# Performance work log

Measured on AMD Instinct MI355X. Metric: run time of the kernel, lower is better.

## Reference

```python
import jax, jax.numpy as jnp
import numpy as np

HEADS = 16
D_MODEL = 1024
GROUP = 4
SEQ = 2048
HEAD_DIM = D_MODEL // HEADS          # 64
KV_HEADS = HEADS // GROUP            # 4


def rope_tables(head_dim, seq_len, base=10000.0):
    # NOTE: faithful to source: exp = -2*arange(0,d,2)/d  (steps of 2 -> base^{-4j/d})
    exp = -2.0 * jnp.arange(0, head_dim, 2, dtype=jnp.float32) / head_dim
    thetas = jnp.power(base, exp)                       # [d/2]
    m = jnp.arange(seq_len, dtype=jnp.float32)          # [S]
    freq = jnp.outer(m, thetas)                         # [S, d/2]
    return jnp.cos(freq), jnp.sin(freq)


def apply_rope(x, cos, sin):
    # x: [B,S,H,D]; complex rotation on consecutive pairs
    B, S, H, D = x.shape
    xr = x.reshape(B, S, H, D // 2, 2)
    x0, x1 = xr[..., 0], xr[..., 1]
    c = cos[None, :S, None, :]
    s = sin[None, :S, None, :]
    out = jnp.stack([x0 * c - x1 * s, x0 * s + x1 * c], axis=-1)
    return out.reshape(B, S, H, D)


def setup_inputs() -> dict:
    key = jax.random.key(0)
    ks = jax.random.split(key, 8)
    B = 1
    q = jax.random.normal(ks[0], (B, SEQ, D_MODEL), dtype=jnp.float32)
    k = jax.random.normal(ks[1], (B, SEQ, D_MODEL), dtype=jnp.float32)
    v = jax.random.normal(ks[2], (B, SEQ, D_MODEL), dtype=jnp.float32)
    mask = jnp.tril(jnp.ones((SEQ, SEQ), dtype=jnp.int32))[None]  # causal [B,S,S]
    sc = 0.02
    Wq = jax.random.normal(ks[3], (D_MODEL, D_MODEL), dtype=jnp.float32) * sc
    Wk = jax.random.normal(ks[4], (D_MODEL, D_MODEL // GROUP), dtype=jnp.float32) * sc
    Wv = jax.random.normal(ks[5], (D_MODEL, D_MODEL // GROUP), dtype=jnp.float32) * sc
    Wo = jax.random.normal(ks[6], (D_MODEL, D_MODEL), dtype=jnp.float32) * sc
    bq = jnp.zeros((D_MODEL,), jnp.float32)
    bk = jnp.zeros((D_MODEL // GROUP,), jnp.float32)
    bv = jnp.zeros((D_MODEL // GROUP,), jnp.float32)
    bo = jnp.zeros((D_MODEL,), jnp.float32)
    return {"q": q, "k": k, "v": v, "mask": mask, "Wq": Wq, "bq": bq,
            "Wk": Wk, "bk": bk, "Wv": Wv, "bv": bv, "Wo": Wo, "bo": bo}


def reference(q, k, v, mask, Wq, bq, Wk, bk, Wv, bv, Wo, bo):
    B, S, _ = q.shape
    cos, sin = rope_tables(HEAD_DIM, S)
    qh = (q @ Wq + bq).reshape(B, S, HEADS, HEAD_DIM)
    kh = (k @ Wk + bk).reshape(B, S, KV_HEADS, HEAD_DIM)
    vh = (v @ Wv + bv).reshape(B, S, KV_HEADS, HEAD_DIM)
    qh = apply_rope(qh, cos, sin)
    kh = apply_rope(kh, cos, sin)
    qh = qh.transpose(0, 2, 1, 3)                       # [B,H,S,D]
    kh = kh.transpose(0, 2, 1, 3)                       # [B,Hkv,S,D]
    vh = vh.transpose(0, 2, 1, 3)
    # torch .repeat tiles: query head j attends kv head j % KV_HEADS
    kh = jnp.tile(kh, (1, GROUP, 1, 1))                 # [B,H,S,D]
    vh = jnp.tile(vh, (1, GROUP, 1, 1))
    scores = jnp.einsum('bhqd,bhkd->bhqk', qh, kh) / jnp.sqrt(
        jnp.asarray(HEAD_DIM, dtype=qh.dtype))
    scores = jnp.where(mask[:, None, :, :] == 0, -jnp.inf, scores)
    attn = jax.nn.softmax(scores, axis=-1)
    out = jnp.einsum('bhqk,bhkd->bhqd', attn, vh)
    out = out.transpose(0, 2, 1, 3).reshape(B, S, D_MODEL)
    return out @ Wo + bo
```

## Files before the change

### kernel.cpp

```cpp
#include <hip/hip_runtime.h>
#include <hip/hip_bf16.h>
#include <math.h>


#define SEQ 2048
#define DM 1024
#define HD 64

using u16 = unsigned short;
typedef __attribute__((ext_vector_type(8))) short bf16x8;
typedef __attribute__((ext_vector_type(4))) float f32x4;

#define QSCALE 0.18033688011112042f

__device__ __forceinline__ u16 f2b(float f) {
    union { float f; unsigned int i; } v; v.f = f;
    unsigned int u = v.i;
    return (u16)((u + 0x7fffu + ((u >> 16) & 1u)) >> 16);
}
__device__ __forceinline__ u16 f2b_fast(float f) {
    union { float f; unsigned int i; } v; v.f = f;
    return (u16)((v.i + 0x8000u) >> 16);
}

__global__ __launch_bounds__(256) void prep_kernel(
    const float* __restrict__ qin, const float* __restrict__ kin, const float* __restrict__ vin,
    const float* __restrict__ Wq, const float* __restrict__ Wk,
    const float* __restrict__ Wv, const float* __restrict__ Wo,
    u16* __restrict__ Xq, u16* __restrict__ Xk, u16* __restrict__ Xv,
    u16* __restrict__ Wt, u16* __restrict__ wot, float2* __restrict__ rope)
{
    const int b = blockIdx.x;
    const int t = threadIdx.x;

    if (b < 640) {
        __shared__ short T[64][72];
        const float* W; u16* dst; int N, t0, rowoff;
        if (b < 256)      { W = Wq; dst = Wt;  N = 1024; t0 = b;       rowoff = 0; }
        else if (b < 320) { W = Wk; dst = Wt;  N = 256;  t0 = b - 256; rowoff = 1024; }
        else if (b < 384) { W = Wv; dst = Wt;  N = 256;  t0 = b - 320; rowoff = 1280; }
        else              { W = Wo; dst = wot; N = 1024; t0 = b - 384; rowoff = 0; }
        const int ntn = N >> 6;
        const int k0 = (t0 / ntn) * 64, n0 = (t0 % ntn) * 64;
        const int r = t >> 4, c4 = (t & 15) * 4;
        #pragma unroll
        for (int rr = 0; rr < 4; ++rr) {
            const int k = r + rr * 16;
            float4 w4 = *reinterpret_cast<const float4*>(W + (size_t)(k0 + k) * N + n0 + c4);
            T[c4 + 0][k] = (short)f2b(w4.x);
            T[c4 + 1][k] = (short)f2b(w4.y);
            T[c4 + 2][k] = (short)f2b(w4.z);
            T[c4 + 3][k] = (short)f2b(w4.w);
        }
        __syncthreads();
        const int n = t >> 2, ck = (t & 3) * 16;
        if (b < 384) {
            const int nt = (rowoff + n0) >> 6, kt = k0 >> 6;
            char* dp = (char*)(dst + (size_t)(nt * 16 + kt) * 4096) + n * 128;
            const int g0 = (t & 3) * 2, rx = n & 7;
            *reinterpret_cast<bf16x8*>(dp + (((g0    ) ^ rx) << 4)) =
                *reinterpret_cast<const bf16x8*>(&T[n][ck]);
            *reinterpret_cast<bf16x8*>(dp + (((g0 + 1) ^ rx) << 4)) =
                *reinterpret_cast<const bf16x8*>(&T[n][ck + 8]);
        } else {
            u16* dp = dst + (size_t)(n0 + n) * DM + k0 + ck;
            *reinterpret_cast<bf16x8*>(dp)     = *reinterpret_cast<const bf16x8*>(&T[n][ck]);
            *reinterpret_cast<bf16x8*>(dp + 8) = *reinterpret_cast<const bf16x8*>(&T[n][ck + 8]);
        }
    } else if (b < 1408) {
        const int idx = b - 640;
        const int which = idx >> 8;
        const int ib = idx & 255;
        const float* src = (which == 0) ? qin : (which == 1) ? kin : vin;
        u16* dst = (which == 0) ? Xq : (which == 1) ? Xk : Xv;
        const int m  = ib * 8 + (t >> 5);
        const int mt = m >> 6, r = m & 63, rx = r & 7;
        const int col0 = (t & 31) * 32;
        const float* sp = src + (size_t)m * 1024 + col0;
        #pragma unroll
        for (int c = 0; c < 4; ++c) {
            float4 x0 = *reinterpret_cast<const float4*>(sp + c * 8);
            float4 x1 = *reinterpret_cast<const float4*>(sp + c * 8 + 4);
            bf16x8 o;
            o[0] = (short)f2b(x0.x); o[1] = (short)f2b(x0.y);
            o[2] = (short)f2b(x0.z); o[3] = (short)f2b(x0.w);
            o[4] = (short)f2b(x1.x); o[5] = (short)f2b(x1.y);
            o[6] = (short)f2b(x1.z); o[7] = (short)f2b(x1.w);
            const int col = col0 + c * 8;
            const int kt = col >> 6, g = (col & 63) >> 3;
            char* dp = (char*)(dst + (size_t)(mt * 16 + kt) * 4096)
                     + r * 128 + ((g ^ rx) << 4);
            *reinterpret_cast<bf16x8*>(dp) = o;
        }
    } else {
        const int m = (b - 1408) * 256 + t;
        float2* rp = rope + (size_t)m * 32;
        for (int pi = 0; pi < 32; ++pi) {
            const float theta = exp2f(-0.8304820237f * (float)pi);
            float sn, cs;
            sincosf((float)m * theta, &sn, &cs);
            rp[pi] = make_float2(cs, sn);
        }
    }
}

__global__ __launch_bounds__(256) void proj_mfma(
    const u16* __restrict__ Xq, const u16* __restrict__ Xk, const u16* __restrict__ Xv,
    const u16* __restrict__ Wt,
    const float* __restrict__ bq, const float* __restrict__ bk, const float* __restrict__ bv,
    const float2* __restrict__ rope,
    u16* __restrict__ Qr, u16* __restrict__ Kr, u16* __restrict__ Vrt)
{
    const int n0 = blockIdx.x * 64, m0 = blockIdx.y * 64;
    const int zone = (n0 < 1024) ? 0 : (n0 < 1280) ? 1 : 2;
    const u16* __restrict__ Az = (zone == 0) ? Xq : (zone == 1) ? Xk : Xv;

    __shared__ __align__(16) u16 As[2][4096];
    __shared__ __align__(16) u16 Bs[2][4096];

    const int t = threadIdx.x;
    const int w = t >> 6, lane = t & 63, lm = lane & 15, quad = lane >> 4;

    f32x4 acc[4] = { {0,0,0,0}, {0,0,0,0}, {0,0,0,0}, {0,0,0,0} };

    const char* Ag = (const char*)(Az + (size_t)(m0 >> 6) * 16 * 4096);
    const char* Bg = (const char*)(Wt + (size_t)(n0 >> 6) * 16 * 4096);

    auto stage = [&](int bufi, int kti) {
        const char* gA = Ag + (size_t)kti * 8192 + w * 2048 + lane * 16;
        const char* gB = Bg + (size_t)kti * 8192 + w * 2048 + lane * 16;
        char* lA = (char*)&As[bufi][0] + w * 2048;
        char* lB = (char*)&Bs[bufi][0] + w * 2048;
        #pragma unroll
        for (int i = 0; i < 2; ++i) {
            __builtin_amdgcn_global_load_lds(
                (const __attribute__((address_space(1))) unsigned int*)(gA + i * 1024),
                (__attribute__((address_space(3))) unsigned int*)(lA + i * 1024), 16, 0, 0);
            __builtin_amdgcn_global_load_lds(
                (const __attribute__((address_space(1))) unsigned int*)(gB + i * 1024),
                (__attribute__((address_space(3))) unsigned int*)(lB + i * 1024), 16, 0, 0);
        }
    };

    stage(0, 0);
    __syncthreads();

    const int rA = 16 * w + lm;
    const int axr = rA & 7;
    for (int kt = 0; kt < 16; ++kt) {
        const int buf = kt & 1;
        if (kt < 15) stage(buf ^ 1, kt + 1);
        const char* Ab = (const char*)&As[buf][0];
        const char* Bb = (const char*)&Bs[buf][0];
        bf16x8 af0 = *reinterpret_cast<const bf16x8*>(Ab + rA * 128 + (((quad    ) ^ axr) << 4));
        bf16x8 af1 = *reinterpret_cast<const bf16x8*>(Ab + rA * 128 + (((4 | quad) ^ axr) << 4));
        #pragma unroll
        for (int nb = 0; nb < 4; ++nb) {
            const int rB = 16 * nb + lm, bxr = rB & 7;
            bf16x8 b0 = *reinterpret_cast<const bf16x8*>(Bb + rB * 128 + (((quad    ) ^ bxr) << 4));
            bf16x8 b1 = *reinterpret_cast<const bf16x8*>(Bb + rB * 128 + (((4 | quad) ^ bxr) << 4));
            acc[nb] = __builtin_amdgcn_mfma_f32_16x16x32_bf16(af0, b0, acc[nb], 0, 0, 0);
            acc[nb] = __builtin_amdgcn_mfma_f32_16x16x32_bf16(af1, b1, acc[nb], 0, 0, 0);
        }
        __syncthreads();
    }

    const float* __restrict__ bias = (zone == 0) ? bq : (zone == 1) ? bk : bv;
    const int nbase = (zone == 0) ? n0 : (zone == 1) ? (n0 - 1024) : (n0 - 1280);
    const int head = nbase >> 6;
    #pragma unroll
    for (int nb = 0; nb < 4; ++nb) {
        const int d = 16 * nb + lm;
        const float bvv = bias[nbase + d];
        float vals[4];
        #pragma unroll
        for (int r = 0; r < 4; ++r) vals[r] = acc[nb][r] + bvv;
        if (zone != 2) {
            const int pi = d >> 1;
            const bool odd = (lm & 1);
            const float sca = (zone == 0) ? QSCALE : 1.0f;
            u16* op = (zone == 0 ? Qr : Kr) + (size_t)head * SEQ * HD;
            #pragma unroll
            for (int r = 0; r < 4; ++r) {
                const int m = m0 + 16 * w + quad * 4 + r;
                const float2 cs2 = rope[(size_t)m * 32 + pi];
                float x  = vals[r];
                float xp = __shfl_xor(x, 1);
                float o  = (odd ? (xp * cs2.y + x * cs2.x)
                                : (x * cs2.x - xp * cs2.y)) * sca;
                op[(size_t)m * HD + d] = f2b(o);
            }
        } else {
            u16* vp = Vrt + ((size_t)head * HD + d) * SEQ;
            #pragma unroll
            for (int r = 0; r < 4; ++r) {
                const int m = m0 + 16 * w + quad * 4 + r;
                const int within = m & 63;
                const int pos = (m & ~63) + 4 * (within & 15) + (within >> 4);
                vp[pos] = f2b(vals[r]);
            }
        }
    }
}

__global__ __launch_bounds__(256) void attn_mfma(
    const u16* __restrict__ Qr, const u16* __restrict__ Kr, const u16* __restrict__ Vrt,
    u16* __restrict__ AO)
{
    const int bid = blockIdx.x;
    const int h  = bid & 15;
    const int qt = (bid < 256) ? (bid >> 4) : 31 - ((bid - 256) >> 4);
    const int kvh = h & 3;

    __shared__ u16 Ks[2][64][72];
    __shared__ u16 Vt[2][64][72];
    __shared__ u16 Ps[4][16][76];

    const int t = threadIdx.x;
    const int w = t >> 6, lane = t & 63, lm = lane & 15, quad = lane >> 4;

    {
        const int row = lane >> 2, c = (lane & 3) * 16;
        const u16* qp = Qr + ((size_t)h * SEQ + qt * 64 + w * 16 + row) * HD + c;
        *reinterpret_cast<bf16x8*>(&Ps[w][row][c])     = *reinterpret_cast<const bf16x8*>(qp);
        *reinterpret_cast<bf16x8*>(&Ps[w][row][c + 8]) = *reinterpret_cast<const bf16x8*>(qp + 8);
    }
    const bf16x8 aq0 = *reinterpret_cast<const bf16x8*>(&Ps[w][lm][quad * 8]);
    const bf16x8 aq1 = *reinterpret_cast<const bf16x8*>(&Ps[w][lm][32 + quad * 8]);

    f32x4 O[4] = { {0,0,0,0}, {0,0,0,0}, {0,0,0,0}, {0,0,0,0} };
    float lp[4] = { 0.f, 0.f, 0.f, 0.f };

    const int srow = t >> 2, sc2 = (t & 3) * 16;
    const u16* kb_ = Kr  + ((size_t)kvh * SEQ + srow) * HD + sc2;
    const u16* vb_ = Vrt + ((size_t)kvh * HD + srow) * SEQ + sc2;
    bf16x8 kR0 = *reinterpret_cast<const bf16x8*>(kb_);
    bf16x8 kR1 = *reinterpret_cast<const bf16x8*>(kb_ + 8);
    bf16x8 vR0 = *reinterpret_cast<const bf16x8*>(vb_);
    bf16x8 vR1 = *reinterpret_cast<const bf16x8*>(vb_ + 8);

    for (int kt = 0; kt <= qt; ++kt) {
        const int buf = kt & 1;
        *reinterpret_cast<bf16x8*>(&Ks[buf][srow][sc2])     = kR0;
        *reinterpret_cast<bf16x8*>(&Ks[buf][srow][sc2 + 8]) = kR1;
        *reinterpret_cast<bf16x8*>(&Vt[buf][srow][sc2])     = vR0;
        *reinterpret_cast<bf16x8*>(&Vt[buf][srow][sc2 + 8]) = vR1;
        if (kt < qt) {
            kR0 = *reinterpret_cast<const bf16x8*>(kb_ + (size_t)(kt + 1) * 64 * HD);
            kR1 = *reinterpret_cast<const bf16x8*>(kb_ + (size_t)(kt + 1) * 64 * HD + 8);
            vR0 = *reinterpret_cast<const bf16x8*>(vb_ + (size_t)(kt + 1) * 64);
            vR1 = *reinterpret_cast<const bf16x8*>(vb_ + (size_t)(kt + 1) * 64 + 8);
        }
        __syncthreads();

        f32x4 s[4];
        #pragma unroll
        for (int nb = 0; nb < 4; ++nb) {
            bf16x8 b0 = *reinterpret_cast<const bf16x8*>(&Ks[buf][16 * nb + lm][quad * 8]);
            bf16x8 b1 = *reinterpret_cast<const bf16x8*>(&Ks[buf][16 * nb + lm][32 + quad * 8]);
            f32x4 zz = { 0.f, 0.f, 0.f, 0.f };
            zz = __builtin_amdgcn_mfma_f32_16x16x32_bf16(aq0, b0, zz, 0, 0, 0);
            s[nb] = __builtin_amdgcn_mfma_f32_16x16x32_bf16(aq1, b1, zz, 0, 0, 0);
        }

        if (kt == qt) {
            #pragma unroll
            for (int nb = 0; nb < 4; ++nb)
                #pragma unroll
                for (int r = 0; r < 4; ++r)
                    if (16 * nb + lm > 16 * w + quad * 4 + r) s[nb][r] = -INFINITY;
        }

        #pragma unroll
        for (int r = 0; r < 4; ++r) {
            u16 pk[4];
            #pragma unroll
            for (int nb = 0; nb < 4; ++nb) {
                float e = __builtin_amdgcn_exp2f(fminf(s[nb][r], 126.f));
                lp[r] += e;
                pk[nb] = f2b_fast(e);
            }
            *reinterpret_cast<uint2*>(&Ps[w][quad * 4 + r][4 * lm]) =
                *reinterpret_cast<uint2*>(pk);
        }

        const bf16x8 ap0 = *reinterpret_cast<const bf16x8*>(&Ps[w][lm][quad * 8]);
        const bf16x8 ap1 = *reinterpret_cast<const bf16x8*>(&Ps[w][lm][32 + quad * 8]);
        #pragma unroll
        for (int db = 0; db < 4; ++db) {
            bf16x8 v0 = *reinterpret_cast<const bf16x8*>(&Vt[buf][16 * db + lm][quad * 8]);
            bf16x8 v1 = *reinterpret_cast<const bf16x8*>(&Vt[buf][16 * db + lm][32 + quad * 8]);
            O[db] = __builtin_amdgcn_mfma_f32_16x16x32_bf16(ap0, v0, O[db], 0, 0, 0);
            O[db] = __builtin_amdgcn_mfma_f32_16x16x32_bf16(ap1, v1, O[db], 0, 0, 0);
        }
    }

    #pragma unroll
    for (int r = 0; r < 4; ++r) {
        #pragma unroll
        for (int off = 1; off < 16; off <<= 1)
            lp[r] += __shfl_xor(lp[r], off);
        const float inv = 1.0f / lp[r];
        const size_t row = (size_t)(qt * 64 + 16 * w + quad * 4 + r) * DM + (size_t)h * HD;
        #pragma unroll
        for (int db = 0; db < 4; ++db)
            AO[row + 16 * db + lm] = f2b(O[db][r] * inv);
    }
}

__global__ __launch_bounds__(256) void oproj_mfma(
    const u16* __restrict__ AO, const u16* __restrict__ wot,
    const float* __restrict__ bo, float* __restrict__ out)
{
    __shared__ short As[2][64][72];
    __shared__ short Bs[2][64][72];
    const int t = threadIdx.x;
    const int w = t >> 6, lane = t & 63, lm = lane & 15, quad = lane >> 4;
    const int m0 = blockIdx.y * 64, n0 = blockIdx.x * 64;
    const int sr = t >> 2, sc = (t & 3) * 16;

    f32x4 acc[4] = { {0,0,0,0}, {0,0,0,0}, {0,0,0,0}, {0,0,0,0} };

    const u16* ap_ = AO  + (size_t)(m0 + sr) * DM + sc;
    const u16* bp_ = wot + (size_t)(n0 + sr) * DM + sc;
    bf16x8 aR0 = *reinterpret_cast<const bf16x8*>(ap_);
    bf16x8 aR1 = *reinterpret_cast<const bf16x8*>(ap_ + 8);
    bf16x8 bR0 = *reinterpret_cast<const bf16x8*>(bp_);
    bf16x8 bR1 = *reinterpret_cast<const bf16x8*>(bp_ + 8);

    for (int k0 = 0; k0 < DM; k0 += 64) {
        const int buf = (k0 >> 6) & 1;
        *reinterpret_cast<bf16x8*>(&As[buf][sr][sc])     = aR0;
        *reinterpret_cast<bf16x8*>(&As[buf][sr][sc + 8]) = aR1;
        *reinterpret_cast<bf16x8*>(&Bs[buf][sr][sc])     = bR0;
        *reinterpret_cast<bf16x8*>(&Bs[buf][sr][sc + 8]) = bR1;
        if (k0 + 64 < DM) {
            aR0 = *reinterpret_cast<const bf16x8*>(ap_ + k0 + 64);
            aR1 = *reinterpret_cast<const bf16x8*>(ap_ + k0 + 72);
            bR0 = *reinterpret_cast<const bf16x8*>(bp_ + k0 + 64);
            bR1 = *reinterpret_cast<const bf16x8*>(bp_ + k0 + 72);
        }
        __syncthreads();
        bf16x8 af0 = *reinterpret_cast<const bf16x8*>(&As[buf][16 * w + lm][quad * 8]);
        bf16x8 af1 = *reinterpret_cast<const bf16x8*>(&As[buf][16 * w + lm][32 + quad * 8]);
        #pragma unroll
        for (int nb = 0; nb < 4; ++nb) {
            bf16x8 b0 = *reinterpret_cast<const bf16x8*>(&Bs[buf][16 * nb + lm][quad * 8]);
            bf16x8 b1 = *reinterpret_cast<const bf16x8*>(&Bs[buf][16 * nb + lm][32 + quad * 8]);
            acc[nb] = __builtin_amdgcn_mfma_f32_16x16x32_bf16(af0, b0, acc[nb], 0, 0, 0);
            acc[nb] = __builtin_amdgcn_mfma_f32_16x16x32_bf16(af1, b1, acc[nb], 0, 0, 0);
        }
        __syncthreads();
    }

    #pragma unroll
    for (int nb = 0; nb < 4; ++nb) {
        const int dl = 16 * nb + lm;
        const float bv = bo[n0 + dl];
        #pragma unroll
        for (int r = 0; r < 4; ++r) {
            const int m = m0 + 16 * w + quad * 4 + r;
            out[(size_t)m * DM + n0 + dl] = acc[nb][r] + bv;
        }
    }
}

extern "C" void kernel_launch(void* const* d_in, const int* in_sizes, int n_in,
                              void* d_out, int out_size, void* d_ws, size_t ws_size,
                              hipStream_t stream)
{
    const float* q  = (const float*)d_in[0];
    const float* k  = (const float*)d_in[1];
    const float* v  = (const float*)d_in[2];
    const float* Wq = (const float*)d_in[4];
    const float* bq = (const float*)d_in[5];
    const float* Wk = (const float*)d_in[6];
    const float* bk = (const float*)d_in[7];
    const float* Wv = (const float*)d_in[8];
    const float* bv = (const float*)d_in[9];
    const float* Wo = (const float*)d_in[10];
    const float* bo = (const float*)d_in[11];
    float* out = (float*)d_out;

    u16* Xq  = (u16*)d_ws;
    u16* Xk  = Xq  + (size_t)SEQ * DM;
    u16* Xv  = Xk  + (size_t)SEQ * DM;
    u16* Wt  = Xv  + (size_t)SEQ * DM;
    u16* wot = Wt  + (size_t)1536 * 1024;
    u16* Qr  = wot + (size_t)1024 * 1024;
    u16* Kr  = Qr  + (size_t)16 * SEQ * HD;
    u16* Vrt = Kr  + (size_t)4 * SEQ * HD;
    u16* AO  = Vrt + (size_t)4 * SEQ * HD;
    float2* rope = (float2*)(AO + (size_t)SEQ * DM);

    hipLaunchKernelGGL(prep_kernel, dim3(1416), dim3(256), 0, stream,
                       q, k, v, Wq, Wk, Wv, Wo, Xq, Xk, Xv, Wt, wot, rope);
    hipLaunchKernelGGL(proj_mfma, dim3(24, 32), dim3(256), 0, stream,
                       Xq, Xk, Xv, Wt, bq, bk, bv, rope, Qr, Kr, Vrt);
    hipLaunchKernelGGL(attn_mfma, dim3(512), dim3(256), 0, stream,
                       Qr, Kr, Vrt, AO);
    hipLaunchKernelGGL(oproj_mfma, dim3(16, 32), dim3(256), 0, stream,
                       AO, wot, bo, out);
}
```

Measured before the change: 165.4 us.

## Fuse four kernels into one persistent kernel with software grid barriers

```diff
diff --git a/kernel.cpp b/kernel.cpp
--- a/kernel.cpp
+++ b/kernel.cpp
@@ -23,344 +23,362 @@
     return (u16)((v.i + 0x8000u) >> 16);
 }
 
-__global__ __launch_bounds__(256) void prep_kernel(
+__device__ __forceinline__ void gbar(unsigned int* bar, int id, int nb) {
+    __syncthreads();
+    if (threadIdx.x == 0) {
+        __threadfence();
+        unsigned int a = atomicAdd(&bar[id], 1u);
+        if (a == (unsigned int)(nb - 1)) {
+            atomicExch(&bar[id + 8], 1u);
+        } else {
+            while (atomicAdd(&bar[id + 8], 0u) == 0u)
+                __builtin_amdgcn_s_sleep(2);
+        }
+        __threadfence();
+    }
+    __syncthreads();
+}
+
+__global__ __launch_bounds__(256) void gqa_fused(
     const float* __restrict__ qin, const float* __restrict__ kin, const float* __restrict__ vin,
     const float* __restrict__ Wq, const float* __restrict__ Wk,
     const float* __restrict__ Wv, const float* __restrict__ Wo,
+    const float* __restrict__ bq, const float* __restrict__ bk,
+    const float* __restrict__ bv, const float* __restrict__ bo,
+    float* __restrict__ out,
     u16* __restrict__ Xq, u16* __restrict__ Xk, u16* __restrict__ Xv,
-    u16* __restrict__ Wt, u16* __restrict__ wot, float2* __restrict__ rope)
+    u16* __restrict__ Wt, u16* __restrict__ wot,
+    u16* __restrict__ Qr, u16* __restrict__ Kr, u16* __restrict__ Vrt,
+    u16* __restrict__ AO, float2* __restrict__ rope, unsigned int* __restrict__ bar)
 {
-    const int b = blockIdx.x;
+    __shared__ __align__(16) char SMEM[46592];
     const int t = threadIdx.x;
-
-    if (b < 640) {
-        __shared__ short T[64][72];
-        const float* W; u16* dst; int N, t0, rowoff;
-        if (b < 256)      { W = Wq; dst = Wt;  N = 1024; t0 = b;       rowoff = 0; }
-        else if (b < 320) { W = Wk; dst = Wt;  N = 256;  t0 = b - 256; rowoff = 1024; }
-        else if (b < 384) { W = Wv; dst = Wt;  N = 256;  t0 = b - 320; rowoff = 1280; }
-        else              { W = Wo; dst = wot; N = 1024; t0 = b - 384; rowoff = 0; }
-        const int ntn = N >> 6;
-        const int k0 = (t0 / ntn) * 64, n0 = (t0 % ntn) * 64;
-        const int r = t >> 4, c4 = (t & 15) * 4;
+    const int NB = gridDim.x;
+
+    {
+        short (*T)[72] = reinterpret_cast<short (*)[72]>(SMEM);
+        for (int b = blockIdx.x; b < 1416; b += NB) {
+            if (b < 640) {
+                const float* W; u16* dst; int N, t0, rowoff;
+                if (b < 256)      { W = Wq; dst = Wt;  N = 1024; t0 = b;       rowoff = 0; }
+                else if (b < 320) { W = Wk; dst = Wt;  N = 256;  t0 = b - 256; rowoff = 1024; }
+                else if (b < 384) { W = Wv; dst = Wt;  N = 256;  t0 = b - 320; rowoff = 1280; }
+                else              { W = Wo; dst = wot; N = 1024; t0 = b - 384; rowoff = 0; }
+                const int ntn = N >> 6;
+                const int k0 = (t0 / ntn) * 64, n0 = (t0 % ntn) * 64;
+                const int r = t >> 4, c4 = (t & 15) * 4;
+                #pragma unroll
+                for (int rr = 0; rr < 4; ++rr) {
+                    const int k = r + rr * 16;
+                    float4 w4 = *reinterpret_cast<const float4*>(W + (size_t)(k0 + k) * N + n0 + c4);
+                    T[c4 + 0][k] = (short)f2b(w4.x);
+                    T[c4 + 1][k] = (short)f2b(w4.y);
+                    T[c4 + 2][k] = (short)f2b(w4.z);
+                    T[c4 + 3][k] = (short)f2b(w4.w);
+                }
+                __syncthreads();
+                const int n = t >> 2, ck = (t & 3) * 16;
+                if (b < 384) {
+                    const int nt = (rowoff + n0) >> 6, kt = k0 >> 6;
+                    char* dp = (char*)(dst + (size_t)(nt * 16 + kt) * 4096) + n * 128;
+                    const int g0 = (t & 3) * 2, rx = n & 7;
+                    *reinterpret_cast<bf16x8*>(dp + (((g0    ) ^ rx) << 4)) =
+                        *reinterpret_cast<const bf16x8*>(&T[n][ck]);
+                    *reinterpret_cast<bf16x8*>(dp + (((g0 + 1) ^ rx) << 4)) =
+                        *reinterpret_cast<const bf16x8*>(&T[n][ck + 8]);
+                } else {
+                    u16* dp = dst + (size_t)(n0 + n) * DM + k0 + ck;
+                    *reinterpret_cast<bf16x8*>(dp)     = *reinterpret_cast<const bf16x8*>(&T[n][ck]);
+                    *reinterpret_cast<bf16x8*>(dp + 8) = *reinterpret_cast<const bf16x8*>(&T[n][ck + 8]);
+                }
+            } else if (b < 1408) {
+                const int idx = b - 640;
+                const int which = idx >> 8;
+                const int ib = idx & 255;
+                const float* src = (which == 0) ? qin : (which == 1) ? kin : vin;
+                u16* dst = (which == 0) ? Xq : (which == 1) ? Xk : Xv;
+                const int m  = ib * 8 + (t >> 5);
+                const int mt = m >> 6, r = m & 63, rx = r & 7;
+                const int col0 = (t & 31) * 32;
+                const float* sp = src + (size_t)m * 1024 + col0;
+                #pragma unroll
+                for (int c = 0; c < 4; ++c) {
+                    float4 x0 = *reinterpret_cast<const float4*>(sp + c * 8);
+                    float4 x1 = *reinterpret_cast<const float4*>(sp + c * 8 + 4);
+                    bf16x8 o;
+                    o[0] = (short)f2b(x0.x); o[1] = (short)f2b(x0.y);
+                    o[2] = (short)f2b(x0.z); o[3] = (short)f2b(x0.w);
+                    o[4] = (short)f2b(x1.x); o[5] = (short)f2b(x1.y);
+                    o[6] = (short)f2b(x1.z); o[7] = (short)f2b(x1.w);
+                    const int col = col0 + c * 8;
+                    const int kt = col >> 6, g = (col & 63) >> 3;
+                    char* dp = (char*)(dst + (size_t)(mt * 16 + kt) * 4096)
+                             + r * 128 + ((g ^ rx) << 4);
+                    *reinterpret_cast<bf16x8*>(dp) = o;
+                }
+            } else {
+                const int m = (b - 1408) * 256 + t;
+                float2* rp = rope + (size_t)m * 32;
+                for (int pi = 0; pi < 32; ++pi) {
+                    const float theta = exp2f(-0.8304820237f * (float)pi);
+                    float sn, cs;
+                    sincosf((float)m * theta, &sn, &cs);
+                    rp[pi] = make_float2(cs, sn);
+                }
+            }
+            __syncthreads();
+        }
+    }
+    gbar(bar, 0, NB);
+
+    {
+        u16 (*As)[4096] = reinterpret_cast<u16 (*)[4096]>(SMEM);
+        u16 (*Bs)[4096] = reinterpret_cast<u16 (*)[4096]>(SMEM + 16384);
+        const int w = t >> 6, lane = t & 63, lm = lane & 15, quad = lane >> 4;
+
+        for (int vb = blockIdx.x; vb < 768; vb += NB) {
+            const int n0 = (vb % 24) * 64, m0 = (vb / 24) * 64;
+            const int zone = (n0 < 1024) ? 0 : (n0 < 1280) ? 1 : 2;
+            const u16* __restrict__ Az = (zone == 0) ? Xq : (zone == 1) ? Xk : Xv;
+
+            f32x4 acc[4] = { {0,0,0,0}, {0,0,0,0}, {0,0,0,0}, {0,0,0,0} };
+
+            const char* Ag = (const char*)(Az + (size_t)(m0 >> 6) * 16 * 4096);
+            const char* Bg = (const char*)(Wt + (size_t)(n0 >> 6) * 16 * 4096);
+
+            auto stage = [&](int bufi, int kti) {
+                const char* gA = Ag + (size_t)kti * 8192 + w * 2048 + lane * 16;
+                const char* gB = Bg + (size_t)kti * 8192 + w * 2048 + lane * 16;
+                char* lA = (char*)&As[bufi][0] + w * 2048;
+                char* lB = (char*)&Bs[bufi][0] + w * 2048;
+                #pragma unroll
+                for (int i = 0; i < 2; ++i) {
+                    __builtin_amdgcn_global_load_lds(
+                        (const __attribute__((address_space(1))) unsigned int*)(gA + i * 1024),
+                        (__attribute__((address_space(3))) unsigned int*)(lA + i * 1024), 16, 0, 0);
+                    __builtin_amdgcn_global_load_lds(
+                        (const __attribute__((address_space(1))) unsigned int*)(gB + i * 1024),
+                        (__attribute__((address_space(3))) unsigned int*)(lB + i * 1024), 16, 0, 0);
+                }
+            };
+
+            stage(0, 0);
+            __syncthreads();
+
+            const int rA = 16 * w + lm;
+            const int axr = rA & 7;
+            for (int kt = 0; kt < 16; ++kt) {
+                const int buf = kt & 1;
+                if (kt < 15) stage(buf ^ 1, kt + 1);
+                const char* Ab = (const char*)&As[buf][0];
+                const char* Bb = (const char*)&Bs[buf][0];
+                bf16x8 af0 = *reinterpret_cast<const bf16x8*>(Ab + rA * 128 + (((quad    ) ^ axr) << 4));
+                bf16x8 af1 = *reinterpret_cast<const bf16x8*>(Ab + rA * 128 + (((4 | quad) ^ axr) << 4));
+                #pragma unroll
+                for (int nb = 0; nb < 4; ++nb) {
+                    const int rB = 16 * nb + lm, bxr = rB & 7;
+                    bf16x8 b0 = *reinterpret_cast<const bf16x8*>(Bb + rB * 128 + (((quad    ) ^ bxr) << 4));
+                    bf16x8 b1 = *reinterpret_cast<const bf16x8*>(Bb + rB * 128 + (((4 | quad) ^ bxr) << 4));
+                    acc[nb] = __builtin_amdgcn_mfma_f32_16x16x32_bf16(af0, b0, acc[nb], 0, 0, 0);
+                    acc[nb] = __builtin_amdgcn_mfma_f32_16x16x32_bf16(af1, b1, acc[nb], 0, 0, 0);
+                }
+                __syncthreads();
+            }
+
+            const float* __restrict__ bias = (zone == 0) ? bq : (zone == 1) ? bk : bv;
+            const int nbase = (zone == 0) ? n0 : (zone == 1) ? (n0 - 1024) : (n0 - 1280);
+            const int head = nbase >> 6;
+            #pragma unroll
+            for (int nb = 0; nb < 4; ++nb) {
+                const int d = 16 * nb + lm;
+                const float bvv = bias[nbase + d];
+                float vals[4];
+                #pragma unroll
+                for (int r = 0; r < 4; ++r) vals[r] = acc[nb][r] + bvv;
+                if (zone != 2) {
+                    const int pi = d >> 1;
+                    const bool odd = (lm & 1);
+                    const float sca = (zone == 0) ? QSCALE : 1.0f;
+                    u16* op = (zone == 0 ? Qr : Kr) + (size_t)head * SEQ * HD;
+                    #pragma unroll
+                    for (int r = 0; r < 4; ++r) {
+                        const int m = m0 + 16 * w + quad * 4 + r;
+                        const float2 cs2 = rope[(size_t)m * 32 + pi];
+                        float x  = vals[r];
+                        float xp = __shfl_xor(x, 1);
+                        float o  = (odd ? (xp * cs2.y + x * cs2.x)
+                                        : (x * cs2.x - xp * cs2.y)) * sca;
+                        op[(size_t)m * HD + d] = f2b(o);
+                    }
+                } else {
+                    u16* vp = Vrt + ((size_t)head * HD + d) * SEQ;
+                    #pragma unroll
+                    for (int r = 0; r < 4; ++r) {
+                        const int m = m0 + 16 * w + quad * 4 + r;
+                        const int within = m & 63;
+                        const int pos = (m & ~63) + 4 * (within & 15) + (within >> 4);
+                        vp[pos] = f2b(vals[r]);
+                    }
+                }
+            }
+            __syncthreads();
+        }
+    }
+    gbar(bar, 1, NB);
+
+    {
+        u16 (*Ks)[64][72] = reinterpret_cast<u16 (*)[64][72]>(SMEM);
+        u16 (*Vt)[64][72] = reinterpret_cast<u16 (*)[64][72]>(SMEM + 18432);
+        u16 (*Ps)[16][76] = reinterpret_cast<u16 (*)[16][76]>(SMEM + 36864);
+
+        const int bid = blockIdx.x;
+        const int h  = bid & 15;
+        const int qt = (bid < 256) ? (bid >> 4) : 31 - ((bid - 256) >> 4);
+        const int kvh = h & 3;
+
+        const int w = t >> 6, lane = t & 63, lm = lane & 15, quad = lane >> 4;
+
+        {
+            const int row = lane >> 2, c = (lane & 3) * 16;
+            const u16* qp = Qr + ((size_t)h * SEQ + qt * 64 + w * 16 + row) * HD + c;
+            *reinterpret_cast<bf16x8*>(&Ps[w][row][c])     = *reinterpret_cast<const bf16x8*>(qp);
+            *reinterpret_cast<bf16x8*>(&Ps[w][row][c + 8]) = *reinterpret_cast<const bf16x8*>(qp + 8);
+        }
+        const bf16x8 aq0 = *reinterpret_cast<const bf16x8*>(&Ps[w][lm][quad * 8]);
+        const bf16x8 aq1 = *reinterpret_cast<const bf16x8*>(&Ps[w][lm][32 + quad * 8]);
+
+        f32x4 O[4] = { {0,0,0,0}, {0,0,0,0}, {0,0,0,0}, {0,0,0,0} };
+        float lp[4] = { 0.f, 0.f, 0.f, 0.f };
+
+        const int srow = t >> 2, sc2 = (t & 3) * 16;
+        const u16* kb_ = Kr  + ((size_t)kvh * SEQ + srow) * HD + sc2;
+        const u16* vb_ = Vrt + ((size_t)kvh * HD + srow) * SEQ + sc2;
+        bf16x8 kR0 = *reinterpret_cast<const bf16x8*>(kb_);
+        bf16x8 kR1 = *reinterpret_cast<const bf16x8*>(kb_ + 8);
+        bf16x8 vR0 = *reinterpret_cast<const bf16x8*>(vb_);
+        bf16x8 vR1 = *reinterpret_cast<const bf16x8*>(vb_ + 8);
+
+        for (int kt = 0; kt <= qt; ++kt) {
+            const int buf = kt & 1;
+            *reinterpret_cast<bf16x8*>(&Ks[buf][srow][sc2])     = kR0;
+            *reinterpret_cast<bf16x8*>(&Ks[buf][srow][sc2 + 8]) = kR1;
+            *reinterpret_cast<bf16x8*>(&Vt[buf][srow][sc2])     = vR0;
+            *reinterpret_cast<bf16x8*>(&Vt[buf][srow][sc2 + 8]) = vR1;
+            if (kt < qt) {
+                kR0 = *reinterpret_cast<const bf16x8*>(kb_ + (size_t)(kt + 1) * 64 * HD);
+                kR1 = *reinterpret_cast<const bf16x8*>(kb_ + (size_t)(kt + 1) * 64 * HD + 8);
+                vR0 = *reinterpret_cast<const bf16x8*>(vb_ + (size_t)(kt + 1) * 64);
+                vR1 = *reinterpret_cast<const bf16x8*>(vb_ + (size_t)(kt + 1) * 64 + 8);
+            }
+            __syncthreads();
+
+            f32x4 s[4];
+            #pragma unroll
+            for (int nb = 0; nb < 4; ++nb) {
+                bf16x8 b0 = *reinterpret_cast<const bf16x8*>(&Ks[buf][16 * nb + lm][quad * 8]);
+                bf16x8 b1 = *reinterpret_cast<const bf16x8*>(&Ks[buf][16 * nb + lm][32 + quad * 8]);
+                f32x4 zz = { 0.f, 0.f, 0.f, 0.f };
+                zz = __builtin_amdgcn_mfma_f32_16x16x32_bf16(aq0, b0, zz, 0, 0, 0);
+                s[nb] = __builtin_amdgcn_mfma_f32_16x16x32_bf16(aq1, b1, zz, 0, 0, 0);
+            }
+
+            if (kt == qt) {
+                #pragma unroll
+                for (int nb = 0; nb < 4; ++nb)
+                    #pragma unroll
+                    for (int r = 0; r < 4; ++r)
+                        if (16 * nb + lm > 16 * w + quad * 4 + r) s[nb][r] = -INFINITY;
+            }
+
+            #pragma unroll
+            for (int r = 0; r < 4; ++r) {
+                u16 pk[4];
+                #pragma unroll
+                for (int nb = 0; nb < 4; ++nb) {
+                    float e = __builtin_amdgcn_exp2f(fminf(s[nb][r], 126.f));
+                    lp[r] += e;
+                    pk[nb] = f2b_fast(e);
+                }
+                *reinterpret_cast<uint2*>(&Ps[w][quad * 4 + r][4 * lm]) =
+                    *reinterpret_cast<uint2*>(pk);
+            }
+
+            const bf16x8 ap0 = *reinterpret_cast<const bf16x8*>(&Ps[w][lm][quad * 8]);
+            const bf16x8 ap1 = *reinterpret_cast<const bf16x8*>(&Ps[w][lm][32 + quad * 8]);
+            #pragma unroll
+            for (int db = 0; db < 4; ++db) {
+                bf16x8 v0 = *reinterpret_cast<const bf16x8*>(&Vt[buf][16 * db + lm][quad * 8]);
+                bf16x8 v1 = *reinterpret_cast<const bf16x8*>(&Vt[buf][16 * db + lm][32 + quad * 8]);
+                O[db] = __builtin_amdgcn_mfma_f32_16x16x32_bf16(ap0, v0, O[db], 0, 0, 0);
+                O[db] = __builtin_amdgcn_mfma_f32_16x16x32_bf16(ap1, v1, O[db], 0, 0, 0);
+            }
+        }
+
         #pragma unroll
-        for (int rr = 0; rr < 4; ++rr) {
-            const int k = r + rr * 16;
-            float4 w4 = *reinterpret_cast<const float4*>(W + (size_t)(k0 + k) * N + n0 + c4);
-            T[c4 + 0][k] = (short)f2b(w4.x);
-            T[c4 + 1][k] = (short)f2b(w4.y);
-            T[c4 + 2][k] = (short)f2b(w4.z);
-            T[c4 + 3][k] = (short)f2b(w4.w);
-        }
-        __syncthreads();
-        const int n = t >> 2, ck = (t & 3) * 16;
-        if (b < 384) {
-            const int nt = (rowoff + n0) >> 6, kt = k0 >> 6;
-            char* dp = (char*)(dst + (size_t)(nt * 16 + kt) * 4096) + n * 128;
-            const int g0 = (t & 3) * 2, rx = n & 7;
-            *reinterpret_cast<bf16x8*>(dp + (((g0    ) ^ rx) << 4)) =
-                *reinterpret_cast<const bf16x8*>(&T[n][ck]);
-            *reinterpret_cast<bf16x8*>(dp + (((g0 + 1) ^ rx) << 4)) =
-                *reinterpret_cast<const bf16x8*>(&T[n][ck + 8]);
-        } else {
-            u16* dp = dst + (size_t)(n0 + n) * DM + k0 + ck;
-            *reinterpret_cast<bf16x8*>(dp)     = *reinterpret_cast<const bf16x8*>(&T[n][ck]);
-            *reinterpret_cast<bf16x8*>(dp + 8) = *reinterpret_cast<const bf16x8*>(&T[n][ck + 8]);
-        }
-    } else if (b < 1408) {
-        const int idx = b - 640;
-        const int which = idx >> 8;
-        const int ib = idx & 255;
-        const float* src = (which == 0) ? qin : (which == 1) ? kin : vin;
-        u16* dst = (which == 0) ? Xq : (which == 1) ? Xk : Xv;
-        const int m  = ib * 8 + (t >> 5);
-        const int mt = m >> 6, r = m & 63, rx = r & 7;
-        const int col0 = (t & 31) * 32;
-        const float* sp = src + (size_t)m * 1024 + col0;
-        #pragma unroll
-        for (int c = 0; c < 4; ++c) {
-            float4 x0 = *reinterpret_cast<const float4*>(sp + c * 8);
-            float4 x1 = *reinterpret_cast<const float4*>(sp + c * 8 + 4);
-            bf16x8 o;
-            o[0] = (short)f2b(x0.x); o[1] = (short)f2b(x0.y);
-            o[2] = (short)f2b(x0.z); o[3] = (short)f2b(x0.w);
-            o[4] = (short)f2b(x1.x); o[5] = (short)f2b(x1.y);
-            o[6] = (short)f2b(x1.z); o[7] = (short)f2b(x1.w);
-            const int col = col0 + c * 8;
-            const int kt = col >> 6, g = (col & 63) >> 3;
-            char* dp = (char*)(dst + (size_t)(mt * 16 + kt) * 4096)
-                     + r * 128 + ((g ^ rx) << 4);
-            *reinterpret_cast<bf16x8*>(dp) = o;
-        }
-    } else {
-        const int m = (b - 1408) * 256 + t;
-        float2* rp = rope + (size_t)m * 32;
-        for (int pi = 0; pi < 32; ++pi) {
-            const float theta = exp2f(-0.8304820237f * (float)pi);
-            float sn, cs;
-            sincosf((float)m * theta, &sn, &cs);
-            rp[pi] = make_float2(cs, sn);
+        for (int r = 0; r < 4; ++r) {
+            #pragma unroll
+            for (int off = 1; off < 16; off <<= 1)
+                lp[r] += __shfl_xor(lp[r], off);
+            const float inv = 1.0f / lp[r];
+            const size_t row = (size_t)(qt * 64 + 16 * w + quad * 4 + r) * DM + (size_t)h * HD;
+            #pragma unroll
+            for (int db = 0; db < 4; ++db)
+                AO[row + 16 * db + lm] = f2b(O[db][r] * inv);
         }
     }
-}
-
-__global__ __launch_bounds__(256) void proj_mfma(
-    const u16* __restrict__ Xq, const u16* __restrict__ Xk, const u16* __restrict__ Xv,
-    const u16* __restrict__ Wt,
-    const float* __restrict__ bq, const float* __restrict__ bk, const float* __restrict__ bv,
-    const float2* __restrict__ rope,
-    u16* __restrict__ Qr, u16* __restrict__ Kr, u16* __restrict__ Vrt)
-{
-    const int n0 = blockIdx.x * 64, m0 = blockIdx.y * 64;
-    const int zone = (n0 < 1024) ? 0 : (n0 < 1280) ? 1 : 2;
-    const u16* __restrict__ Az = (zone == 0) ? Xq : (zone == 1) ? Xk : Xv;
-
-    __shared__ __align__(16) u16 As[2][4096];
-    __shared__ __align__(16) u16 Bs[2][4096];
-
-    const int t = threadIdx.x;
-    const int w = t >> 6, lane = t & 63, lm = lane & 15, quad = lane >> 4;
-
-    f32x4 acc[4] = { {0,0,0,0}, {0,0,0,0}, {0,0,0,0}, {0,0,0,0} };
-
-    const char* Ag = (const char*)(Az + (size_t)(m0 >> 6) * 16 * 4096);
-    const char* Bg = (const char*)(Wt + (size_t)(n0 >> 6) * 16 * 4096);
-
-    auto stage = [&](int bufi, int kti) {
-        const char* gA = Ag + (size_t)kti * 8192 + w * 2048 + lane * 16;
-        const char* gB = Bg + (size_t)kti * 8192 + w * 2048 + lane * 16;
-        char* lA = (char*)&As[bufi][0] + w * 2048;
-        char* lB = (char*)&Bs[bufi][0] + w * 2048;
-        #pragma unroll
-        for (int i = 0; i < 2; ++i) {
-            __builtin_amdgcn_global_load_lds(
-                (const __attribute__((address_space(1))) unsigned int*)(gA + i * 1024),
-                (__attribute__((address_space(3))) unsigned int*)(lA + i * 1024), 16, 0, 0);
-            __builtin_amdgcn_global_load_lds(
-                (const __attribute__((address_space(1))) unsigned int*)(gB + i * 1024),
-                (__attribute__((address_space(3))) unsigned int*)(lB + i * 1024), 16, 0, 0);
-        }
-    };
-
-    stage(0, 0);
-    __syncthreads();
-
-    const int rA = 16 * w + lm;
-    const int axr = rA & 7;
-    for (int kt = 0; kt < 16; ++kt) {
-        const int buf = kt & 1;
-        if (kt < 15) stage(buf ^ 1, kt + 1);
-        const char* Ab = (const char*)&As[buf][0];
-        const char* Bb = (const char*)&Bs[buf][0];
-        bf16x8 af0 = *reinterpret_cast<const bf16x8*>(Ab + rA * 128 + (((quad    ) ^ axr) << 4));
-        bf16x8 af1 = *reinterpret_cast<const bf16x8*>(Ab + rA * 128 + (((4 | quad) ^ axr) << 4));
+    gbar(bar, 2, NB);
+
+    {
+        short (*As)[64][72] = reinterpret_cast<short (*)[64][72]>(SMEM);
+        short (*Bs)[64][72] = reinterpret_cast<short (*)[64][72]>(SMEM + 18432);
+        const int w = t >> 6, lane = t & 63, lm = lane & 15, quad = lane >> 4;
+        const int vb = blockIdx.x;
+        const int n0 = (vb & 15) * 64, m0 = (vb >> 4) * 64;
+        const int sr = t >> 2, sc = (t & 3) * 16;
+
+        f32x4 acc[4] = { {0,0,0,0}, {0,0,0,0}, {0,0,0,0}, {0,0,0,0} };
+
+        const u16* ap_ = AO  + (size_t)(m0 + sr) * DM + sc;
+        const u16* bp_ = wot + (size_t)(n0 + sr) * DM + sc;
+        bf16x8 aR0 = *reinterpret_cast<const bf16x8*>(ap_);
+        bf16x8 aR1 = *reinterpret_cast<const bf16x8*>(ap_ + 8);
+        bf16x8 bR0 = *reinterpret_cast<const bf16x8*>(bp_);
+        bf16x8 bR1 = *reinterpret_cast<const bf16x8*>(bp_ + 8);
+
+        for (int k0 = 0; k0 < DM; k0 += 64) {
+            const int buf = (k0 >> 6) & 1;
+            *reinterpret_cast<bf16x8*>(&As[buf][sr][sc])     = aR0;
+            *reinterpret_cast<bf16x8*>(&As[buf][sr][sc + 8]) = aR1;
+            *reinterpret_cast<bf16x8*>(&Bs[buf][sr][sc])     = bR0;
+            *reinterpret_cast<bf16x8*>(&Bs[buf][sr][sc + 8]) = bR1;
+            if (k0 + 64 < DM) {
+                aR0 = *reinterpret_cast<const bf16x8*>(ap_ + k0 + 64);
+                aR1 = *reinterpret_cast<const bf16x8*>(ap_ + k0 + 72);
+                bR0 = *reinterpret_cast<const bf16x8*>(bp_ + k0 + 64);
+                bR1 = *reinterpret_cast<const bf16x8*>(bp_ + k0 + 72);
+            }
+            __syncthreads();
+            bf16x8 af0 = *reinterpret_cast<const bf16x8*>(&As[buf][16 * w + lm][quad * 8]);
+            bf16x8 af1 = *reinterpret_cast<const bf16x8*>(&As[buf][16 * w + lm][32 + quad * 8]);
+            #pragma unroll
+            for (int nb = 0; nb < 4; ++nb) {
+                bf16x8 b0 = *reinterpret_cast<const bf16x8*>(&Bs[buf][16 * nb + lm][quad * 8]);
+                bf16x8 b1 = *reinterpret_cast<const bf16x8*>(&Bs[buf][16 * nb + lm][32 + quad * 8]);
+                acc[nb] = __builtin_amdgcn_mfma_f32_16x16x32_bf16(af0, b0, acc[nb], 0, 0, 0);
+                acc[nb] = __builtin_amdgcn_mfma_f32_16x16x32_bf16(af1, b1, acc[nb], 0, 0, 0);
+            }
+            __syncthreads();
+        }
+
         #pragma unroll
         for (int nb = 0; nb < 4; ++nb) {
-            const int rB = 16 * nb + lm, bxr = rB & 7;
-            bf16x8 b0 = *reinterpret_cast<const bf16x8*>(Bb + rB * 128 + (((quad    ) ^ bxr) << 4));
-            bf16x8 b1 = *reinterpret_cast<const bf16x8*>(Bb + rB * 128 + (((4 | quad) ^ bxr) << 4));
-            acc[nb] = __builtin_amdgcn_mfma_f32_16x16x32_bf16(af0, b0, acc[nb], 0, 0, 0);
-            acc[nb] = __builtin_amdgcn_mfma_f32_16x16x32_bf16(af1, b1, acc[nb], 0, 0, 0);
-        }
-        __syncthreads();
-    }
-
-    const float* __restrict__ bias = (zone == 0) ? bq : (zone == 1) ? bk : bv;
-    const int nbase = (zone == 0) ? n0 : (zone == 1) ? (n0 - 1024) : (n0 - 1280);
-    const int head = nbase >> 6;
-    #pragma unroll
-    for (int nb = 0; nb < 4; ++nb) {
-        const int d = 16 * nb + lm;
-        const float bvv = bias[nbase + d];
-        float vals[4];
-        #pragma unroll
-        for (int r = 0; r < 4; ++r) vals[r] = acc[nb][r] + bvv;
-        if (zone != 2) {
-            const int pi = d >> 1;
-            const bool odd = (lm & 1);
-            const float sca = (zone == 0) ? QSCALE : 1.0f;
-            u16* op = (zone == 0 ? Qr : Kr) + (size_t)head * SEQ * HD;
+            const int dl = 16 * nb + lm;
+            const float bv2 = bo[n0 + dl];
             #pragma unroll
             for (int r = 0; r < 4; ++r) {
                 const int m = m0 + 16 * w + quad * 4 + r;
-                const float2 cs2 = rope[(size_t)m * 32 + pi];
-                float x  = vals[r];
-                float xp = __shfl_xor(x, 1);
-                float o  = (odd ? (xp * cs2.y + x * cs2.x)
-                                : (x * cs2.x - xp * cs2.y)) * sca;
-                op[(size_t)m * HD + d] = f2b(o);
-            }
-        } else {
-            u16* vp = Vrt + ((size_t)head * HD + d) * SEQ;
-            #pragma unroll
-            for (int r = 0; r < 4; ++r) {
-                const int m = m0 + 16 * w + quad * 4 + r;
-                const int within = m & 63;
-                const int pos = (m & ~63) + 4 * (within & 15) + (within >> 4);
-                vp[pos] = f2b(vals[r]);
-            }
-        }
-    }
-}
-
-__global__ __launch_bounds__(256) void attn_mfma(
-    const u16* __restrict__ Qr, const u16* __restrict__ Kr, const u16* __restrict__ Vrt,
-    u16* __restrict__ AO)
-{
-    const int bid = blockIdx.x;
-    const int h  = bid & 15;
-    const int qt = (bid < 256) ? (bid >> 4) : 31 - ((bid - 256) >> 4);
-    const int kvh = h & 3;
-
-    __shared__ u16 Ks[2][64][72];
-    __shared__ u16 Vt[2][64][72];
-    __shared__ u16 Ps[4][16][76];
-
-    const int t = threadIdx.x;
-    const int w = t >> 6, lane = t & 63, lm = lane & 15, quad = lane >> 4;
-
-    {
-        const int row = lane >> 2, c = (lane & 3) * 16;
-        const u16* qp = Qr + ((size_t)h * SEQ + qt * 64 + w * 16 + row) * HD + c;
-        *reinterpret_cast<bf16x8*>(&Ps[w][row][c])     = *reinterpret_cast<const bf16x8*>(qp);
-        *reinterpret_cast<bf16x8*>(&Ps[w][row][c + 8]) = *reinterpret_cast<const bf16x8*>(qp + 8);
-    }
-    const bf16x8 aq0 = *reinterpret_cast<const bf16x8*>(&Ps[w][lm][quad * 8]);
-    const bf16x8 aq1 = *reinterpret_cast<const bf16x8*>(&Ps[w][lm][32 + quad * 8]);
-
-    f32x4 O[4] = { {0,0,0,0}, {0,0,0,0}, {0,0,0,0}, {0,0,0,0} };
-    float lp[4] = { 0.f, 0.f, 0.f, 0.f };
-
-    const int srow = t >> 2, sc2 = (t & 3) * 16;
-    const u16* kb_ = Kr  + ((size_t)kvh * SEQ + srow) * HD + sc2;
-    const u16* vb_ = Vrt + ((size_t)kvh * HD + srow) * SEQ + sc2;
-    bf16x8 kR0 = *reinterpret_cast<const bf16x8*>(kb_);
-    bf16x8 kR1 = *reinterpret_cast<const bf16x8*>(kb_ + 8);
-    bf16x8 vR0 = *reinterpret_cast<const bf16x8*>(vb_);
-    bf16x8 vR1 = *reinterpret_cast<const bf16x8*>(vb_ + 8);
-
-    for (int kt = 0; kt <= qt; ++kt) {
-        const int buf = kt & 1;
-        *reinterpret_cast<bf16x8*>(&Ks[buf][srow][sc2])     = kR0;
-        *reinterpret_cast<bf16x8*>(&Ks[buf][srow][sc2 + 8]) = kR1;
-        *reinterpret_cast<bf16x8*>(&Vt[buf][srow][sc2])     = vR0;
-        *reinterpret_cast<bf16x8*>(&Vt[buf][srow][sc2 + 8]) = vR1;
-        if (kt < qt) {
-            kR0 = *reinterpret_cast<const bf16x8*>(kb_ + (size_t)(kt + 1) * 64 * HD);
-            kR1 = *reinterpret_cast<const bf16x8*>(kb_ + (size_t)(kt + 1) * 64 * HD + 8);
-            vR0 = *reinterpret_cast<const bf16x8*>(vb_ + (size_t)(kt + 1) * 64);
-            vR1 = *reinterpret_cast<const bf16x8*>(vb_ + (size_t)(kt + 1) * 64 + 8);
-        }
-        __syncthreads();
-
-        f32x4 s[4];
-        #pragma unroll
-        for (int nb = 0; nb < 4; ++nb) {
-            bf16x8 b0 = *reinterpret_cast<const bf16x8*>(&Ks[buf][16 * nb + lm][quad * 8]);
-            bf16x8 b1 = *reinterpret_cast<const bf16x8*>(&Ks[buf][16 * nb + lm][32 + quad * 8]);
-            f32x4 zz = { 0.f, 0.f, 0.f, 0.f };
-            zz = __builtin_amdgcn_mfma_f32_16x16x32_bf16(aq0, b0, zz, 0, 0, 0);
-            s[nb] = __builtin_amdgcn_mfma_f32_16x16x32_bf16(aq1, b1, zz, 0, 0, 0);
-        }
-
-        if (kt == qt) {
-            #pragma unroll
-            for (int nb = 0; nb < 4; ++nb)
-                #pragma unroll
-                for (int r = 0; r < 4; ++r)
-                    if (16 * nb + lm > 16 * w + quad * 4 + r) s[nb][r] = -INFINITY;
-        }
-
-        #pragma unroll
-        for (int r = 0; r < 4; ++r) {
-            u16 pk[4];
-            #pragma unroll
-            for (int nb = 0; nb < 4; ++nb) {
-                float e = __builtin_amdgcn_exp2f(fminf(s[nb][r], 126.f));
-                lp[r] += e;
-                pk[nb] = f2b_fast(e);
-            }
-            *reinterpret_cast<uint2*>(&Ps[w][quad * 4 + r][4 * lm]) =
-                *reinterpret_cast<uint2*>(pk);
-        }
-
-        const bf16x8 ap0 = *reinterpret_cast<const bf16x8*>(&Ps[w][lm][quad * 8]);
-        const bf16x8 ap1 = *reinterpret_cast<const bf16x8*>(&Ps[w][lm][32 + quad * 8]);
-        #pragma unroll
-        for (int db = 0; db < 4; ++db) {
-            bf16x8 v0 = *reinterpret_cast<const bf16x8*>(&Vt[buf][16 * db + lm][quad * 8]);
-            bf16x8 v1 = *reinterpret_cast<const bf16x8*>(&Vt[buf][16 * db + lm][32 + quad * 8]);
-            O[db] = __builtin_amdgcn_mfma_f32_16x16x32_bf16(ap0, v0, O[db], 0, 0, 0);
-            O[db] = __builtin_amdgcn_mfma_f32_16x16x32_bf16(ap1, v1, O[db], 0, 0, 0);
-        }
-    }
-
-    #pragma unroll
-    for (int r = 0; r < 4; ++r) {
-        #pragma unroll
-        for (int off = 1; off < 16; off <<= 1)
-            lp[r] += __shfl_xor(lp[r], off);
-        const float inv = 1.0f / lp[r];
-        const size_t row = (size_t)(qt * 64 + 16 * w + quad * 4 + r) * DM + (size_t)h * HD;
-        #pragma unroll
-        for (int db = 0; db < 4; ++db)
-            AO[row + 16 * db + lm] = f2b(O[db][r] * inv);
-    }
-}
-
-__global__ __launch_bounds__(256) void oproj_mfma(
-    const u16* __restrict__ AO, const u16* __restrict__ wot,
-    const float* __restrict__ bo, float* __restrict__ out)
-{
-    __shared__ short As[2][64][72];
-    __shared__ short Bs[2][64][72];
-    const int t = threadIdx.x;
-    const int w = t >> 6, lane = t & 63, lm = lane & 15, quad = lane >> 4;
-    const int m0 = blockIdx.y * 64, n0 = blockIdx.x * 64;
-    const int sr = t >> 2, sc = (t & 3) * 16;
-
-    f32x4 acc[4] = { {0,0,0,0}, {0,0,0,0}, {0,0,0,0}, {0,0,0,0} };
-
-    const u16* ap_ = AO  + (size_t)(m0 + sr) * DM + sc;
-    const u16* bp_ = wot + (size_t)(n0 + sr) * DM + sc;
-    bf16x8 aR0 = *reinterpret_cast<const bf16x8*>(ap_);
-    bf16x8 aR1 = *reinterpret_cast<const bf16x8*>(ap_ + 8);
-    bf16x8 bR0 = *reinterpret_cast<const bf16x8*>(bp_);
-    bf16x8 bR1 = *reinterpret_cast<const bf16x8*>(bp_ + 8);
-
-    for (int k0 = 0; k0 < DM; k0 += 64) {
-        const int buf = (k0 >> 6) & 1;
-        *reinterpret_cast<bf16x8*>(&As[buf][sr][sc])     = aR0;
-        *reinterpret_cast<bf16x8*>(&As[buf][sr][sc + 8]) = aR1;
-        *reinterpret_cast<bf16x8*>(&Bs[buf][sr][sc])     = bR0;
-        *reinterpret_cast<bf16x8*>(&Bs[buf][sr][sc + 8]) = bR1;
-        if (k0 + 64 < DM) {
-            aR0 = *reinterpret_cast<const bf16x8*>(ap_ + k0 + 64);
-            aR1 = *reinterpret_cast<const bf16x8*>(ap_ + k0 + 72);
-            bR0 = *reinterpret_cast<const bf16x8*>(bp_ + k0 + 64);
-            bR1 = *reinterpret_cast<const bf16x8*>(bp_ + k0 + 72);
-        }
-        __syncthreads();
-        bf16x8 af0 = *reinterpret_cast<const bf16x8*>(&As[buf][16 * w + lm][quad * 8]);
-        bf16x8 af1 = *reinterpret_cast<const bf16x8*>(&As[buf][16 * w + lm][32 + quad * 8]);
-        #pragma unroll
-        for (int nb = 0; nb < 4; ++nb) {
-            bf16x8 b0 = *reinterpret_cast<const bf16x8*>(&Bs[buf][16 * nb + lm][quad * 8]);
-            bf16x8 b1 = *reinterpret_cast<const bf16x8*>(&Bs[buf][16 * nb + lm][32 + quad * 8]);
-            acc[nb] = __builtin_amdgcn_mfma_f32_16x16x32_bf16(af0, b0, acc[nb], 0, 0, 0);
-            acc[nb] = __builtin_amdgcn_mfma_f32_16x16x32_bf16(af1, b1, acc[nb], 0, 0, 0);
-        }
-        __syncthreads();
-    }
-
-    #pragma unroll
-    for (int nb = 0; nb < 4; ++nb) {
-        const int dl = 16 * nb + lm;
-        const float bv = bo[n0 + dl];
-        #pragma unroll
-        for (int r = 0; r < 4; ++r) {
-            const int m = m0 + 16 * w + quad * 4 + r;
-            out[(size_t)m * DM + n0 + dl] = acc[nb][r] + bv;
+                out[(size_t)m * DM + n0 + dl] = acc[nb][r] + bv2;
+            }
         }
     }
 }
@@ -392,13 +410,21 @@
     u16* Vrt = Kr  + (size_t)4 * SEQ * HD;
     u16* AO  = Vrt + (size_t)4 * SEQ * HD;
     float2* rope = (float2*)(AO + (size_t)SEQ * DM);
-
-    hipLaunchKernelGGL(prep_kernel, dim3(1416), dim3(256), 0, stream,
-                       q, k, v, Wq, Wk, Wv, Wo, Xq, Xk, Xv, Wt, wot, rope);
-    hipLaunchKernelGGL(proj_mfma, dim3(24, 32), dim3(256), 0, stream,
-                       Xq, Xk, Xv, Wt, bq, bk, bv, rope, Qr, Kr, Vrt);
-    hipLaunchKernelGGL(attn_mfma, dim3(512), dim3(256), 0, stream,
-                       Qr, Kr, Vrt, AO);
-    hipLaunchKernelGGL(oproj_mfma, dim3(16, 32), dim3(256), 0, stream,
-                       AO, wot, bo, out);
+    unsigned int* bar = (unsigned int*)((char*)d_ws + ((size_t)32 << 20));
+
+    hipMemsetAsync(bar, 0, 64, stream);
+
+    void* args[] = {
+        (void*)&q, (void*)&k, (void*)&v,
+        (void*)&Wq, (void*)&Wk, (void*)&Wv, (void*)&Wo,
+        (void*)&bq, (void*)&bk, (void*)&bv, (void*)&bo,
+        (void*)&out,
+        (void*)&Xq, (void*)&Xk, (void*)&Xv, (void*)&Wt, (void*)&wot,
+        (void*)&Qr, (void*)&Kr, (void*)&Vrt, (void*)&AO, (void*)&rope,
+        (void*)&bar
+    };
+    hipLaunchKernelGGL(gqa_fused, dim3(512), dim3(256), 0, stream,
+                       q, k, v, Wq, Wk, Wv, Wo, bq, bk, bv, bo, out,
+                       Xq, Xk, Xv, Wt, wot, Qr, Kr, Vrt, AO, rope, bar);
+    (void)args;
 }
```

After: 363.1 us. +119.5%, slower.
